# Performance work log

Hardware: AMD Instinct MI355X
Metric: run time of the kernel (lower is better)

The kernel has to match this reference:

```python
import jax, jax.numpy as jnp
import numpy as np

N_NODES = 50000
N_EDGES = 800000
D_IN = 512
D_OUT = 512


def setup_inputs() -> dict:
    key = jax.random.key(0)
    k1, k2, k3, k4, k5 = jax.random.split(key, 5)
    adj_rows = jnp.sort(jax.random.randint(k1, (N_EDGES,), 0, N_NODES, dtype=jnp.int32))
    adj_cols = jax.random.randint(k2, (N_EDGES,), 0, N_NODES, dtype=jnp.int32)
    adj_vals = jax.random.uniform(k3, (N_EDGES,), dtype=jnp.float32)
    u_f = jax.random.normal(k4, (N_NODES, D_IN), dtype=jnp.float32)
    # xavier_uniform init for weight [in_feats, out_feats]
    limit = float(np.sqrt(6.0 / (D_IN + D_OUT)))
    weight = jax.random.uniform(k5, (D_IN, D_OUT), dtype=jnp.float32, minval=-limit, maxval=limit)
    return {"adj_rows": adj_rows, "adj_cols": adj_cols, "adj_vals": adj_vals,
            "u_f": u_f, "weight": weight}


def reference(adj_rows, adj_cols, adj_vals, u_f, weight):
    # dense projection: [N, d_in] @ [d_in, d_out] -> [N, d_out]
    h = u_f @ weight
    # sparse adj (COO) @ h: gather source rows, scale by edge vals, scatter-add to dest rows
    msgs = adj_vals[:, None] * h[adj_cols]              # [E, d_out]
    out = jax.ops.segment_sum(msgs, adj_rows, num_segments=N_NODES)  # [N, d_out]
    return jax.nn.relu(out)
```

## Files before the change

kernel.cpp:

```cpp
#include <hip/hip_runtime.h>
#include <cstdint>
#include <cstddef>

#define N_NODES 50000
#define N_EDGES 800000
#define D 512
#define M_PAD 50048

typedef __bf16 bf16x8 __attribute__((ext_vector_type(8)));
typedef float floatx4 __attribute__((ext_vector_type(4)));

typedef const __attribute__((address_space(1))) unsigned int* gas_u32p;
typedef __attribute__((address_space(3))) unsigned int* las_u32p;

__device__ __forceinline__ unsigned short f2bf(float f) {
    unsigned int u = __builtin_bit_cast(unsigned int, f);
    u += 0x7FFFu + ((u >> 16) & 1u);
    return (unsigned short)(u >> 16);
}
__device__ __forceinline__ float bflo(unsigned int u) {
    return __builtin_bit_cast(float, u << 16);
}
__device__ __forceinline__ float bfhi(unsigned int u) {
    return __builtin_bit_cast(float, u & 0xFFFF0000u);
}
__device__ __forceinline__ bf16x8 cvt8f(floatx4 lo, floatx4 hi) {
    bf16x8 r;
    r[0] = (__bf16)lo[0]; r[1] = (__bf16)lo[1]; r[2] = (__bf16)lo[2]; r[3] = (__bf16)lo[3];
    r[4] = (__bf16)hi[0]; r[5] = (__bf16)hi[1]; r[6] = (__bf16)hi[2]; r[7] = (__bf16)hi[3];
    return r;
}

__global__ __launch_bounds__(256) void k_convert_wt(const float* __restrict__ w,
                                                    unsigned short* __restrict__ wt) {
    int id = blockIdx.x * 256 + threadIdx.x;
    int n = id >> 9, k = id & 511;
    wt[id] = f2bf(w[k * D + n]);
}

__global__ __launch_bounds__(256) void k_rowptr(const int* __restrict__ rows,
                                                int* __restrict__ rp) {
    int i = blockIdx.x * 256 + threadIdx.x;
    if (i > N_NODES) return;
    int lo = 0, hi = N_EDGES;
    while (lo < hi) {
        int mid = (lo + hi) >> 1;
        if (rows[mid] < i) lo = mid + 1; else hi = mid;
    }
    rp[i] = lo;
}

__global__ __launch_bounds__(256) void k_gemm(const float* __restrict__ Af,
                                              const unsigned short* __restrict__ WT,
                                              unsigned short* __restrict__ H) {
    __shared__ float          lAf[128 * 32];
    __shared__ unsigned short lB [128 * 32];
    int b = blockIdx.x;
    int mt, nt;
    if (b < 1536) {
        mt = (b >> 5) * 8 + (b & 7);
        nt = (b >> 3) & 3;
    } else {
        int r = b - 1536;
        mt = 384 + (r % 7);
        nt = r / 7;
    }
    const int tid  = threadIdx.x;
    const int wave = tid >> 6, lane = tid & 63;
    const int tileM0 = mt * 128;
    const int tileN0 = nt * 128;
    const int wr = wave >> 1, wc = wave & 1;

    const int lrowA  = lane >> 3;
    const int lslotA = lane & 7;
    int asrc[4];
#pragma unroll
    for (int g = 0; g < 4; g++) {
        int m  = wave * 32 + g * 8 + lrowA;
        int gm = tileM0 + m;
        if (gm > N_NODES - 1) gm = N_NODES - 1;
        int c = lslotA ^ (m & 7);
        asrc[g] = gm * D + c * 4;
    }

    const int lrowB = lane >> 2, lslotB = lane & 3;
    const int r0 = wave * 32;
    const int m0 = r0 + lrowB,      m1 = r0 + 16 + lrowB;
    const int q0 = (lslotB - (m0 >> 1)) & 3;
    const int q1 = (lslotB - (m1 >> 1)) & 3;
    const unsigned short* gB0 = WT + (size_t)(tileN0 + m0) * D + q0 * 8;
    const unsigned short* gB1 = WT + (size_t)(tileN0 + m1) * D + q1 * 8;
    unsigned short* lB0 = lB + r0 * 32;
    unsigned short* lB1 = lB + (r0 + 16) * 32;

    floatx4 acc[4][4] = {};

    const int quad = lane >> 4, half = lane & 15;
    int offAlo[4], offAhi[4], offB[4];
#pragma unroll
    for (int i = 0; i < 4; i++) {
        int m = wr * 64 + i * 16 + half;
        offAlo[i] = m * 32 + (((quad * 2)     ^ (m & 7)) * 4);
        offAhi[i] = m * 32 + (((quad * 2 + 1) ^ (m & 7)) * 4);
        int n = wc * 64 + i * 16 + half;
        offB[i] = n * 32 + ((quad + (n >> 1)) & 3) * 8;
    }

    for (int k0 = 0; k0 < D; k0 += 32) {
        __syncthreads();
#pragma unroll
        for (int g = 0; g < 4; g++)
            __builtin_amdgcn_global_load_lds((gas_u32p)(Af + asrc[g] + k0),
                                             (las_u32p)(lAf + (wave * 32 + g * 8) * 32), 16, 0, 0);
        __builtin_amdgcn_global_load_lds((gas_u32p)(gB0 + k0), (las_u32p)lB0, 16, 0, 0);
        __builtin_amdgcn_global_load_lds((gas_u32p)(gB1 + k0), (las_u32p)lB1, 16, 0, 0);
        __syncthreads();

        bf16x8 af[4], bfr[4];
#pragma unroll
        for (int i = 0; i < 4; i++) {
            floatx4 lo = *(const floatx4*)(lAf + offAlo[i]);
            floatx4 hi = *(const floatx4*)(lAf + offAhi[i]);
            af[i]  = cvt8f(lo, hi);
            bfr[i] = *(const bf16x8*)(lB + offB[i]);
        }
#pragma unroll
        for (int i = 0; i < 4; i++)
#pragma unroll
            for (int j = 0; j < 4; j++)
                acc[i][j] = __builtin_amdgcn_mfma_f32_16x16x32_bf16(af[i], bfr[j], acc[i][j], 0, 0, 0);
    }

#pragma unroll
    for (int i = 0; i < 4; i++) {
        int gm0 = tileM0 + wr * 64 + i * 16 + quad * 4;
#pragma unroll
        for (int j = 0; j < 4; j++) {
            int gn = tileN0 + wc * 64 + j * 16 + half;
#pragma unroll
            for (int r = 0; r < 4; r++) {
                H[(size_t)(gm0 + r) * D + gn] = f2bf(acc[i][j][r]);
            }
        }
    }
}

__global__ __launch_bounds__(256) void k_scatter(const int* __restrict__ rp,
                                                 const int* __restrict__ cols,
                                                 const float* __restrict__ vals,
                                                 const unsigned short* __restrict__ H,
                                                 float* __restrict__ out) {
    int node = (int)((blockIdx.x * 256 + threadIdx.x) >> 6);
    int lane = threadIdx.x & 63;
    if (node >= N_NODES) return;
    int s = rp[node], e = rp[node + 1];
    float a0 = 0.f, a1 = 0.f, a2 = 0.f, a3 = 0.f;
    float a4 = 0.f, a5 = 0.f, a6 = 0.f, a7 = 0.f;
    const uint4* H4 = (const uint4*)H;
    const int lq = lane;
    for (int t = s; t < e; t += 4) {
        int last = e - 1;
        int t1 = t + 1 < e ? t + 1 : last;
        int t2 = t + 2 < e ? t + 2 : last;
        int t3 = t + 3 < e ? t + 3 : last;
        int c0 = cols[t],  c1 = cols[t1], c2 = cols[t2], c3 = cols[t3];
        float v0 = vals[t];
        float v1 = t + 1 < e ? vals[t1] : 0.f;
        float v2 = t + 2 < e ? vals[t2] : 0.f;
        float v3 = t + 3 < e ? vals[t3] : 0.f;
        uint4 d0 = H4[(size_t)c0 * 64 + lq];
        uint4 d1 = H4[(size_t)c1 * 64 + lq];
        uint4 d2 = H4[(size_t)c2 * 64 + lq];
        uint4 d3 = H4[(size_t)c3 * 64 + lq];
        a0 = fmaf(v0, bflo(d0.x), a0); a1 = fmaf(v0, bfhi(d0.x), a1);
        a2 = fmaf(v0, bflo(d0.y), a2); a3 = fmaf(v0, bfhi(d0.y), a3);
        a4 = fmaf(v0, bflo(d0.z), a4); a5 = fmaf(v0, bfhi(d0.z), a5);
        a6 = fmaf(v0, bflo(d0.w), a6); a7 = fmaf(v0, bfhi(d0.w), a7);
        a0 = fmaf(v1, bflo(d1.x), a0); a1 = fmaf(v1, bfhi(d1.x), a1);
        a2 = fmaf(v1, bflo(d1.y), a2); a3 = fmaf(v1, bfhi(d1.y), a3);
        a4 = fmaf(v1, bflo(d1.z), a4); a5 = fmaf(v1, bfhi(d1.z), a5);
        a6 = fmaf(v1, bflo(d1.w), a6); a7 = fmaf(v1, bfhi(d1.w), a7);
        a0 = fmaf(v2, bflo(d2.x), a0); a1 = fmaf(v2, bfhi(d2.x), a1);
        a2 = fmaf(v2, bflo(d2.y), a2); a3 = fmaf(v2, bfhi(d2.y), a3);
        a4 = fmaf(v2, bflo(d2.z), a4); a5 = fmaf(v2, bfhi(d2.z), a5);
        a6 = fmaf(v2, bflo(d2.w), a6); a7 = fmaf(v2, bfhi(d2.w), a7);
        a0 = fmaf(v3, bflo(d3.x), a0); a1 = fmaf(v3, bfhi(d3.x), a1);
        a2 = fmaf(v3, bflo(d3.y), a2); a3 = fmaf(v3, bfhi(d3.y), a3);
        a4 = fmaf(v3, bflo(d3.z), a4); a5 = fmaf(v3, bfhi(d3.z), a5);
        a6 = fmaf(v3, bflo(d3.w), a6); a7 = fmaf(v3, bfhi(d3.w), a7);
    }
    float* o = out + (size_t)node * D + (size_t)lane * 8;
    *(float4*)o       = make_float4(fmaxf(a0, 0.f), fmaxf(a1, 0.f), fmaxf(a2, 0.f), fmaxf(a3, 0.f));
    *(float4*)(o + 4) = make_float4(fmaxf(a4, 0.f), fmaxf(a5, 0.f), fmaxf(a6, 0.f), fmaxf(a7, 0.f));
}

extern "C" void kernel_launch(void* const* d_in, const int* in_sizes, int n_in,
                              void* d_out, int out_size, void* d_ws, size_t ws_size,
                              hipStream_t stream) {
    const int*   adj_rows = (const int*)d_in[0];
    const int*   adj_cols = (const int*)d_in[1];
    const float* adj_vals = (const float*)d_in[2];
    const float* u_f      = (const float*)d_in[3];
    const float* weight   = (const float*)d_in[4];
    float* out = (float*)d_out;

    char* ws = (char*)d_ws;
    unsigned short* wt_bf = (unsigned short*)ws;
    unsigned short* h_bf  = (unsigned short*)(ws + 524288);
    int* rowptr           = (int*)(ws + 524288 + 51249152);

    hipLaunchKernelGGL(k_convert_wt, dim3(1024),  dim3(256), 0, stream, weight, wt_bf);
    hipLaunchKernelGGL(k_rowptr,     dim3(196),   dim3(256), 0, stream, adj_rows, rowptr);
    hipLaunchKernelGGL(k_gemm,       dim3(1564),  dim3(256), 0, stream, u_f, wt_bf, h_bf);
    hipLaunchKernelGGL(k_scatter,    dim3(12500), dim3(256), 0, stream, rowptr, adj_cols, adj_vals, h_bf, out);
}
```

Before: 195.9 us.

## Double-buffer GEMM LDS staging and merge prep kernels into one launch

The GEMM now stages the next K-slice into a second LDS buffer while the current slice feeds the MFMAs. It uses partial vmcnt waits and raw s_barrier in place of two __syncthreads per iteration. The weight-transpose and rowptr kernels are merged into a single launch to remove one kernel dispatch. LDS use doubles, which may reduce occupancy, and the hand-written waitcnt counts must match the number of issued loads.

```diff
diff --git a/kernel.cpp b/kernel.cpp
--- a/kernel.cpp
+++ b/kernel.cpp
@@ -31,30 +31,32 @@
     return r;
 }
 
-__global__ __launch_bounds__(256) void k_convert_wt(const float* __restrict__ w,
-                                                    unsigned short* __restrict__ wt) {
-    int id = blockIdx.x * 256 + threadIdx.x;
-    int n = id >> 9, k = id & 511;
-    wt[id] = f2bf(w[k * D + n]);
-}
-
-__global__ __launch_bounds__(256) void k_rowptr(const int* __restrict__ rows,
-                                                int* __restrict__ rp) {
-    int i = blockIdx.x * 256 + threadIdx.x;
-    if (i > N_NODES) return;
-    int lo = 0, hi = N_EDGES;
-    while (lo < hi) {
-        int mid = (lo + hi) >> 1;
-        if (rows[mid] < i) lo = mid + 1; else hi = mid;
-    }
-    rp[i] = lo;
+__global__ __launch_bounds__(256) void k_prep(const float* __restrict__ w,
+                                              unsigned short* __restrict__ wt,
+                                              const int* __restrict__ rows,
+                                              int* __restrict__ rp) {
+    int blk = blockIdx.x;
+    if (blk < 1024) {
+        int id = blk * 256 + threadIdx.x;
+        int n = id >> 9, k = id & 511;
+        wt[id] = f2bf(w[k * D + n]);
+    } else {
+        int i = (blk - 1024) * 256 + threadIdx.x;
+        if (i > N_NODES) return;
+        int lo = 0, hi = N_EDGES;
+        while (lo < hi) {
+            int mid = (lo + hi) >> 1;
+            if (rows[mid] < i) lo = mid + 1; else hi = mid;
+        }
+        rp[i] = lo;
+    }
 }
 
 __global__ __launch_bounds__(256) void k_gemm(const float* __restrict__ Af,
                                               const unsigned short* __restrict__ WT,
                                               unsigned short* __restrict__ H) {
-    __shared__ float          lAf[128 * 32];
-    __shared__ unsigned short lB [128 * 32];
+    __shared__ float          lAf[2 * 128 * 32];
+    __shared__ unsigned short lB [2 * 128 * 32];
     int b = blockIdx.x;
     int mt, nt;
     if (b < 1536) {
@@ -90,8 +92,6 @@
     const int q1 = (lslotB - (m1 >> 1)) & 3;
     const unsigned short* gB0 = WT + (size_t)(tileN0 + m0) * D + q0 * 8;
     const unsigned short* gB1 = WT + (size_t)(tileN0 + m1) * D + q1 * 8;
-    unsigned short* lB0 = lB + r0 * 32;
-    unsigned short* lB1 = lB + (r0 + 16) * 32;
 
     floatx4 acc[4][4] = {};
 
@@ -106,29 +106,46 @@
         offB[i] = n * 32 + ((quad + (n >> 1)) & 3) * 8;
     }
 
-    for (int k0 = 0; k0 < D; k0 += 32) {
-        __syncthreads();
+    auto stage = [&](int buf, int k0) {
+        float*          dA = lAf + buf * 4096;
+        unsigned short* dB = lB  + buf * 4096;
 #pragma unroll
         for (int g = 0; g < 4; g++)
             __builtin_amdgcn_global_load_lds((gas_u32p)(Af + asrc[g] + k0),
-                                             (las_u32p)(lAf + (wave * 32 + g * 8) * 32), 16, 0, 0);
-        __builtin_amdgcn_global_load_lds((gas_u32p)(gB0 + k0), (las_u32p)lB0, 16, 0, 0);
-        __builtin_amdgcn_global_load_lds((gas_u32p)(gB1 + k0), (las_u32p)lB1, 16, 0, 0);
-        __syncthreads();
-
+                                             (las_u32p)(dA + (wave * 32 + g * 8) * 32), 16, 0, 0);
+        __builtin_amdgcn_global_load_lds((gas_u32p)(gB0 + k0), (las_u32p)(dB + r0 * 32), 16, 0, 0);
+        __builtin_amdgcn_global_load_lds((gas_u32p)(gB1 + k0), (las_u32p)(dB + (r0 + 16) * 32), 16, 0, 0);
+    };
+
+    stage(0, 0);
+    for (int kk = 0; kk < 16; kk++) {
+        const int cur = kk & 1;
+        if (kk < 15) {
+            stage(cur ^ 1, (kk + 1) * 32);
+            asm volatile("s_waitcnt vmcnt(6)" ::: "memory");
+        } else {
+            asm volatile("s_waitcnt vmcnt(0)" ::: "memory");
+        }
+        __builtin_amdgcn_s_barrier();
+
+        const float*          cA = lAf + cur * 4096;
+        const unsigned short* cB = lB  + cur * 4096;
         bf16x8 af[4], bfr[4];
 #pragma unroll
         for (int i = 0; i < 4; i++) {
-            floatx4 lo = *(const floatx4*)(lAf + offAlo[i]);
-            floatx4 hi = *(const floatx4*)(lAf + offAhi[i]);
+            floatx4 lo = *(const floatx4*)(cA + offAlo[i]);
+            floatx4 hi = *(const floatx4*)(cA + offAhi[i]);
             af[i]  = cvt8f(lo, hi);
-            bfr[i] = *(const bf16x8*)(lB + offB[i]);
+            bfr[i] = *(const bf16x8*)(cB + offB[i]);
         }
 #pragma unroll
         for (int i = 0; i < 4; i++)
 #pragma unroll
             for (int j = 0; j < 4; j++)
                 acc[i][j] = __builtin_amdgcn_mfma_f32_16x16x32_bf16(af[i], bfr[j], acc[i][j], 0, 0, 0);
+
+        asm volatile("s_waitcnt lgkmcnt(0)" ::: "memory");
+        __builtin_amdgcn_s_barrier();
     }
 
 #pragma unroll
@@ -209,8 +226,7 @@
     unsigned short* h_bf  = (unsigned short*)(ws + 524288);
     int* rowptr           = (int*)(ws + 524288 + 51249152);
 
-    hipLaunchKernelGGL(k_convert_wt, dim3(1024),  dim3(256), 0, stream, weight, wt_bf);
-    hipLaunchKernelGGL(k_rowptr,     dim3(196),   dim3(256), 0, stream, adj_rows, rowptr);
-    hipLaunchKernelGGL(k_gemm,       dim3(1564),  dim3(256), 0, stream, u_f, wt_bf, h_bf);
-    hipLaunchKernelGGL(k_scatter,    dim3(12500), dim3(256), 0, stream, rowptr, adj_cols, adj_vals, h_bf, out);
-}
+    hipLaunchKernelGGL(k_prep,    dim3(1220),  dim3(256), 0, stream, weight, wt_bf, adj_rows, rowptr);
+    hipLaunchKernelGGL(k_gemm,    dim3(1564),  dim3(256), 0, stream, u_f, wt_bf, h_bf);
+    hipLaunchKernelGGL(k_scatter, dim3(12500), dim3(256), 0, stream, rowptr, adj_cols, adj_vals, h_bf, out);
+}
```

Result: no change. 195.9 us (+0.0%).

## Slice scatter by feature columns per XCD and merge prep kernels

Applied to the files above, without the earlier changes.

Merges the weight-transpose and rowptr kernels into one launch. Restructures the SpMM gather so each wave handles 16 nodes, with each node covering a 32-column slice of H. Slices are assigned to XCDs by block index, so each XCD's L2 only holds its own column slices of H. Adds nontemporal loads for cols/vals and nontemporal stores for the output. In exchange, the index and value arrays are re-read once per slice, and the edge loop is no longer unrolled by 4.

```diff
diff --git a/kernel.cpp b/kernel.cpp
--- a/kernel.cpp
+++ b/kernel.cpp
@@ -31,23 +31,25 @@
     return r;
 }
 
-__global__ __launch_bounds__(256) void k_convert_wt(const float* __restrict__ w,
-                                                    unsigned short* __restrict__ wt) {
-    int id = blockIdx.x * 256 + threadIdx.x;
-    int n = id >> 9, k = id & 511;
-    wt[id] = f2bf(w[k * D + n]);
-}
-
-__global__ __launch_bounds__(256) void k_rowptr(const int* __restrict__ rows,
-                                                int* __restrict__ rp) {
-    int i = blockIdx.x * 256 + threadIdx.x;
-    if (i > N_NODES) return;
-    int lo = 0, hi = N_EDGES;
-    while (lo < hi) {
-        int mid = (lo + hi) >> 1;
-        if (rows[mid] < i) lo = mid + 1; else hi = mid;
-    }
-    rp[i] = lo;
+__global__ __launch_bounds__(256) void k_prep(const float* __restrict__ w,
+                                              unsigned short* __restrict__ wt,
+                                              const int* __restrict__ rows,
+                                              int* __restrict__ rp) {
+    int blk = blockIdx.x;
+    if (blk < 1024) {
+        int id = blk * 256 + threadIdx.x;
+        int n = id >> 9, k = id & 511;
+        wt[id] = f2bf(w[k * D + n]);
+    } else {
+        int i = (blk - 1024) * 256 + threadIdx.x;
+        if (i > N_NODES) return;
+        int lo = 0, hi = N_EDGES;
+        while (lo < hi) {
+            int mid = (lo + hi) >> 1;
+            if (rows[mid] < i) lo = mid + 1; else hi = mid;
+        }
+        rp[i] = lo;
+    }
 }
 
 __global__ __launch_bounds__(256) void k_gemm(const float* __restrict__ Af,
@@ -145,53 +147,43 @@
     }
 }
 
+#define SBLK 784
 __global__ __launch_bounds__(256) void k_scatter(const int* __restrict__ rp,
                                                  const int* __restrict__ cols,
                                                  const float* __restrict__ vals,
                                                  const unsigned short* __restrict__ H,
                                                  float* __restrict__ out) {
-    int node = (int)((blockIdx.x * 256 + threadIdx.x) >> 6);
-    int lane = threadIdx.x & 63;
+    int b    = blockIdx.x;
+    int xcd  = b & 7;
+    int j    = b >> 3;
+    int phase = (j >= SBLK) ? 1 : 0;
+    int slice = xcd * 2 + phase;
+    int sblk  = j - phase * SBLK;
+    int wid   = sblk * 4 + (threadIdx.x >> 6);
+    int lane  = threadIdx.x & 63;
+    int nsub  = lane >> 2;
+    int q     = lane & 3;
+    int node  = wid * 16 + nsub;
     if (node >= N_NODES) return;
+
     int s = rp[node], e = rp[node + 1];
+    const uint4* Hs = (const uint4*)H + slice * 4 + q;
     float a0 = 0.f, a1 = 0.f, a2 = 0.f, a3 = 0.f;
     float a4 = 0.f, a5 = 0.f, a6 = 0.f, a7 = 0.f;
-    const uint4* H4 = (const uint4*)H;
-    const int lq = lane;
-    for (int t = s; t < e; t += 4) {
-        int last = e - 1;
-        int t1 = t + 1 < e ? t + 1 : last;
-        int t2 = t + 2 < e ? t + 2 : last;
-        int t3 = t + 3 < e ? t + 3 : last;
-        int c0 = cols[t],  c1 = cols[t1], c2 = cols[t2], c3 = cols[t3];
-        float v0 = vals[t];
-        float v1 = t + 1 < e ? vals[t1] : 0.f;
-        float v2 = t + 2 < e ? vals[t2] : 0.f;
-        float v3 = t + 3 < e ? vals[t3] : 0.f;
-        uint4 d0 = H4[(size_t)c0 * 64 + lq];
-        uint4 d1 = H4[(size_t)c1 * 64 + lq];
-        uint4 d2 = H4[(size_t)c2 * 64 + lq];
-        uint4 d3 = H4[(size_t)c3 * 64 + lq];
-        a0 = fmaf(v0, bflo(d0.x), a0); a1 = fmaf(v0, bfhi(d0.x), a1);
-        a2 = fmaf(v0, bflo(d0.y), a2); a3 = fmaf(v0, bfhi(d0.y), a3);
-        a4 = fmaf(v0, bflo(d0.z), a4); a5 = fmaf(v0, bfhi(d0.z), a5);
-        a6 = fmaf(v0, bflo(d0.w), a6); a7 = fmaf(v0, bfhi(d0.w), a7);
-        a0 = fmaf(v1, bflo(d1.x), a0); a1 = fmaf(v1, bfhi(d1.x), a1);
-        a2 = fmaf(v1, bflo(d1.y), a2); a3 = fmaf(v1, bfhi(d1.y), a3);
-        a4 = fmaf(v1, bflo(d1.z), a4); a5 = fmaf(v1, bfhi(d1.z), a5);
-        a6 = fmaf(v1, bflo(d1.w), a6); a7 = fmaf(v1, bfhi(d1.w), a7);
-        a0 = fmaf(v2, bflo(d2.x), a0); a1 = fmaf(v2, bfhi(d2.x), a1);
-        a2 = fmaf(v2, bflo(d2.y), a2); a3 = fmaf(v2, bfhi(d2.y), a3);
-        a4 = fmaf(v2, bflo(d2.z), a4); a5 = fmaf(v2, bfhi(d2.z), a5);
-        a6 = fmaf(v2, bflo(d2.w), a6); a7 = fmaf(v2, bfhi(d2.w), a7);
-        a0 = fmaf(v3, bflo(d3.x), a0); a1 = fmaf(v3, bfhi(d3.x), a1);
-        a2 = fmaf(v3, bflo(d3.y), a2); a3 = fmaf(v3, bfhi(d3.y), a3);
-        a4 = fmaf(v3, bflo(d3.z), a4); a5 = fmaf(v3, bfhi(d3.z), a5);
-        a6 = fmaf(v3, bflo(d3.w), a6); a7 = fmaf(v3, bfhi(d3.w), a7);
-    }
-    float* o = out + (size_t)node * D + (size_t)lane * 8;
-    *(float4*)o       = make_float4(fmaxf(a0, 0.f), fmaxf(a1, 0.f), fmaxf(a2, 0.f), fmaxf(a3, 0.f));
-    *(float4*)(o + 4) = make_float4(fmaxf(a4, 0.f), fmaxf(a5, 0.f), fmaxf(a6, 0.f), fmaxf(a7, 0.f));
+    for (int t = s; t < e; ++t) {
+        int   c = __builtin_nontemporal_load(cols + t);
+        float v = __builtin_nontemporal_load(vals + t);
+        uint4 d = Hs[(size_t)c * 64];
+        a0 = fmaf(v, bflo(d.x), a0); a1 = fmaf(v, bfhi(d.x), a1);
+        a2 = fmaf(v, bflo(d.y), a2); a3 = fmaf(v, bfhi(d.y), a3);
+        a4 = fmaf(v, bflo(d.z), a4); a5 = fmaf(v, bfhi(d.z), a5);
+        a6 = fmaf(v, bflo(d.w), a6); a7 = fmaf(v, bfhi(d.w), a7);
+    }
+    float* o = out + (size_t)node * D + slice * 32 + q * 8;
+    floatx4 r0 = { fmaxf(a0, 0.f), fmaxf(a1, 0.f), fmaxf(a2, 0.f), fmaxf(a3, 0.f) };
+    floatx4 r1 = { fmaxf(a4, 0.f), fmaxf(a5, 0.f), fmaxf(a6, 0.f), fmaxf(a7, 0.f) };
+    __builtin_nontemporal_store(r0, (floatx4*)o);
+    __builtin_nontemporal_store(r1, (floatx4*)(o + 4));
 }
 
 extern "C" void kernel_launch(void* const* d_in, const int* in_sizes, int n_in,
@@ -209,8 +201,7 @@
     unsigned short* h_bf  = (unsigned short*)(ws + 524288);
     int* rowptr           = (int*)(ws + 524288 + 51249152);
 
-    hipLaunchKernelGGL(k_convert_wt, dim3(1024),  dim3(256), 0, stream, weight, wt_bf);
-    hipLaunchKernelGGL(k_rowptr,     dim3(196),   dim3(256), 0, stream, adj_rows, rowptr);
-    hipLaunchKernelGGL(k_gemm,       dim3(1564),  dim3(256), 0, stream, u_f, wt_bf, h_bf);
-    hipLaunchKernelGGL(k_scatter,    dim3(12500), dim3(256), 0, stream, rowptr, adj_cols, adj_vals, h_bf, out);
-}
+    hipLaunchKernelGGL(k_prep,    dim3(1220),      dim3(256), 0, stream, weight, wt_bf, adj_rows, rowptr);
+    hipLaunchKernelGGL(k_gemm,    dim3(1564),      dim3(256), 0, stream, u_f, wt_bf, h_bf);
+    hipLaunchKernelGGL(k_scatter, dim3(16 * SBLK), dim3(256), 0, stream, rowptr, adj_cols, adj_vals, h_bf, out);
+}
```

Result: slower. 501.7 us (+156.1%).
